# Kernel tuning notes

Hardware: AMD Instinct MI355X
Metric: run time of the kernel (lower is better)

Reference implementation:

```python
import jax, jax.numpy as jnp
import numpy as np
from math import sqrt

D_MODEL = 1024
D_HEAD = 128
TAU = 30.0
B, L = 8, 2048


def setup_inputs() -> dict:
    key = jax.random.key(0)
    k1, k2, k3, k4 = jax.random.split(key, 4)
    x = jax.random.normal(k1, (B, L, D_MODEL), dtype=jnp.float32)
    attention_mask = jnp.ones((B, L), dtype=jnp.int32)
    W_Q = jax.random.normal(k2, (D_HEAD, D_MODEL), dtype=jnp.float32)
    W_K = jax.random.normal(k3, (D_HEAD, D_MODEL), dtype=jnp.float32)
    W_V = jax.random.normal(k4, (D_HEAD, D_MODEL), dtype=jnp.float32)
    return {"input": x, "attention_mask": attention_mask, "W_Q": W_Q, "W_K": W_K, "W_V": W_V}


def reference(input, attention_mask, W_Q, W_K, W_V):
    # Single-head projections: [B, L, d_head]
    Q = input @ W_Q.T
    K = input @ W_K.T
    V = input @ W_V.T
    # Scaled scores: [B, L, L]
    S = jnp.einsum("bqd,bkd->bqk", Q, K) / sqrt(D_HEAD)
    # tanh soft-capping (mode == 'tanh-clipped')
    S = TAU * jnp.tanh(S)
    l = input.shape[1]
    # causal mask: strictly upper triangle -> -inf
    causal = jnp.triu(jnp.ones((l, l), dtype=bool), k=1)
    S = jnp.where(causal[None, :, :], -jnp.inf, S)
    # padding mask on keys: [B, 1, L]
    S = jnp.where(attention_mask[:, None, :] == 0, -jnp.inf, S)
    Attn = jax.nn.softmax(S, axis=-1)
    return Attn @ V
```

## Files before the change

### kernel.cpp

```cpp
#include <hip/hip_runtime.h>
#include <hip/hip_bf16.h>

#define BATCH  8
#define SEQ    2048
#define DMODEL 1024
#define DHEAD  128

typedef __attribute__((ext_vector_type(4))) float f32x4;
typedef __attribute__((ext_vector_type(4))) float f4;
typedef _Float16 f16;
typedef __attribute__((ext_vector_type(8))) _Float16 f16x8;
typedef __attribute__((ext_vector_type(8))) __bf16 bf16x8;
typedef __attribute__((ext_vector_type(16))) unsigned short u16x16;

__device__ __forceinline__ unsigned short f2bf(float f) {
    unsigned u = __builtin_bit_cast(unsigned, f);
    u += 0x7fffu + ((u >> 16) & 1u);
    return (unsigned short)(u >> 16);
}

#if __has_builtin(__builtin_amdgcn_exp2f)
#define EXP2(x) __builtin_amdgcn_exp2f(x)
#else
#define EXP2(x) exp2f(x)
#endif

__device__ __forceinline__ float fast_rcp(float x) {
#if __has_builtin(__builtin_amdgcn_rcpf)
    return __builtin_amdgcn_rcpf(x);
#else
    return 1.0f / x;
#endif
}

__device__ __forceinline__ void async_copy16(const void* g, void* l) {
    __builtin_amdgcn_global_load_lds(
        (const __attribute__((address_space(1))) unsigned int*)g,
        (__attribute__((address_space(3))) unsigned int*)l,
        16, 0, 0);
}

__global__ __launch_bounds__(256) void wsplit_kernel(
    const float* __restrict__ WQ, const float* __restrict__ WK,
    const float* __restrict__ WV, f16* __restrict__ Wsp)
{
    const int gid = blockIdx.x * 256 + threadIdx.x;
    const int row = gid & 127;
    const int hi  = (gid >> 7) & 3;
    const int ks  = (gid >> 9) & 31;
    const int mat = gid >> 14;
    const float* W = (mat < 2) ? WQ : (mat < 4) ? WK : WV;
    const float* src = W + (size_t)row * DMODEL + ks * 32 + hi * 8;
    f4 v0 = *(const f4*)src, v1 = *(const f4*)(src + 4);
    const bool lopart = (mat == 1 || mat == 3);
    f16x8 o;
    #pragma unroll
    for (int j = 0; j < 4; ++j) {
        f16 h0 = (f16)v0[j], h1 = (f16)v1[j];
        o[j]     = lopart ? (f16)(v0[j] - (float)h0) : h0;
        o[j + 4] = lopart ? (f16)(v1[j] - (float)h1) : h1;
    }
    *reinterpret_cast<f16x8*>(Wsp + (size_t)gid * 8) = o;
}

__global__ __launch_bounds__(256) void proj_kernel(
    const float* __restrict__ x, const f16* __restrict__ Wsp,
    f16* __restrict__ Qh, f16* __restrict__ Ql,
    f16* __restrict__ Kh, f16* __restrict__ Kl,
    unsigned short* __restrict__ Vtb)
{
    __shared__ float Xs[2][64][32];
    __shared__ f16 Wl[2][5][4][64][8];

    const int tid  = threadIdx.x;
    const int lane = tid & 63;
    const int w    = tid >> 6;
    const int lo   = lane & 15;
    const int hi   = lane >> 4;
    const int m0   = blockIdx.x * 64;
    const int bn   = blockIdx.y;

    f32x4 accQ[4] = {}, accK[4] = {}, accV[4] = {};

    const int r0 = (w * 2 + 0) * 8 + (lane >> 3);
    const int r1 = (w * 2 + 1) * 8 + (lane >> 3);
    const float* xsrc0 = x + (size_t)(m0 + r0) * DMODEL + (((lane & 7) ^ (r0 & 7)) << 2);
    const float* xsrc1 = x + (size_t)(m0 + r1) * DMODEL + (((lane & 7) ^ (r1 & 7)) << 2);
    const f16* wsrc0 = Wsp + (size_t)(w * 128 + bn * 64 + lane) * 8;

    auto stageX = [&](int ks, int buf) {
        async_copy16(xsrc0 + ks * 32, &Xs[buf][(w * 2 + 0) * 8][0]);
        async_copy16(xsrc1 + ks * 32, &Xs[buf][(w * 2 + 1) * 8][0]);
    };
    auto stageW = [&](int ks, int buf) {
        #pragma unroll
        for (int m = 0; m < 5; ++m)
            async_copy16(wsrc0 + (size_t)(m * 32 + ks) * 4096,
                         &Wl[buf][m][w][0][0]);
    };

    stageX(0, 0);
    stageW(0, 0);
    __syncthreads();

    for (int ks = 0; ks < 32; ++ks) {
        const int cur = ks & 1;
        if (ks < 31) { stageX(ks + 1, cur ^ 1); stageW(ks + 1, cur ^ 1); }

        f16x8 W5[5];
        #pragma unroll
        for (int m = 0; m < 5; ++m)
            W5[m] = *reinterpret_cast<const f16x8*>(&Wl[cur][m][hi][w * 16 + lo][0]);

        #pragma unroll
        for (int rb = 0; rb < 4; ++rb) {
            const int row = rb * 16 + lo;
            const float* xr = &Xs[cur][row][0];
            f4 a0 = *(const f4*)(xr + (((2 * hi)     ^ (row & 7)) << 2));
            f4 a1 = *(const f4*)(xr + (((2 * hi + 1) ^ (row & 7)) << 2));
            f16x8 ah, al;
            #pragma unroll
            for (int j = 0; j < 4; ++j) {
                f16 h0 = (f16)a0[j]; ah[j]     = h0; al[j]     = (f16)(a0[j] - (float)h0);
                f16 h1 = (f16)a1[j]; ah[j + 4] = h1; al[j + 4] = (f16)(a1[j] - (float)h1);
            }
            accQ[rb] = __builtin_amdgcn_mfma_f32_16x16x32_f16(ah, W5[0], accQ[rb], 0, 0, 0);
            accQ[rb] = __builtin_amdgcn_mfma_f32_16x16x32_f16(ah, W5[1], accQ[rb], 0, 0, 0);
            accQ[rb] = __builtin_amdgcn_mfma_f32_16x16x32_f16(al, W5[0], accQ[rb], 0, 0, 0);
            accK[rb] = __builtin_amdgcn_mfma_f32_16x16x32_f16(ah, W5[2], accK[rb], 0, 0, 0);
            accK[rb] = __builtin_amdgcn_mfma_f32_16x16x32_f16(ah, W5[3], accK[rb], 0, 0, 0);
            accK[rb] = __builtin_amdgcn_mfma_f32_16x16x32_f16(al, W5[2], accK[rb], 0, 0, 0);
            accV[rb] = __builtin_amdgcn_mfma_f32_16x16x32_f16(ah, W5[4], accV[rb], 0, 0, 0);
        }
        __syncthreads();
    }

    #pragma unroll
    for (int rb = 0; rb < 4; ++rb)
        #pragma unroll
        for (int r = 0; r < 4; ++r) {
            const int m = m0 + rb * 16 + hi * 4 + r;
            const int n = bn * 64 + w * 16 + lo;
            const size_t idx = (size_t)m * DHEAD + n;
            float vq = accQ[rb][r];
            f16 hq = (f16)vq;
            Qh[idx] = hq; Ql[idx] = (f16)(vq - (float)hq);
            float vk = accK[rb][r];
            f16 hk = (f16)vk;
            Kh[idx] = hk; Kl[idx] = (f16)(vk - (float)hk);
            const int bb = m >> 11, l = m & 2047;
            Vtb[((size_t)bb * DHEAD + n) * SEQ + l] = f2bf(accV[rb][r]);
        }
}

#define PART_STRIDE 8256
__global__ __launch_bounds__(512) void attn_kernel(
    const f16* __restrict__ Qh, const f16* __restrict__ Ql,
    const f16* __restrict__ Kh, const f16* __restrict__ Kl,
    const unsigned short* __restrict__ Vtb, const int* __restrict__ mask,
    float* __restrict__ part)
{
    __shared__ f16 Khs[2][64][136];
    __shared__ f16 Kls[2][64][136];
    __shared__ unsigned short Vs[2][128][72];
    __shared__ int Ms[2][64];
    __shared__ unsigned short Plds[8][16][40];

    const int tid  = threadIdx.x;
    const int lane = tid & 63;
    const int w    = tid >> 6;
    const int lo   = lane & 15;
    const int hi   = lane >> 4;
    const int wq   = w & 3;
    const int wk   = w >> 2;
    const int b    = blockIdx.x;
    const int qs   = 31 - (int)blockIdx.y;
    const int z    = blockIdx.z;
    const int qrow = qs * 64 + wq * 16;

    const float c2p = 0.25506061907448296f;
    const float c1  = -86.561702453337804f;

    f16x8 qh[4], ql[4];
    {
        const size_t off = ((size_t)(b * SEQ + qrow + lo)) * DHEAD + hi * 8;
        #pragma unroll
        for (int c = 0; c < 4; ++c) {
            qh[c] = *reinterpret_cast<const f16x8*>(Qh + off + c * 32);
            ql[c] = *reinterpret_cast<const f16x8*>(Ql + off + c * 32);
        }
    }

    const int krow = tid >> 3;
    const int kcol = (tid & 7) * 16;
    const int vrow = tid >> 2;
    const int vcol = (tid & 3) * 16;

    f16x8  rKh0, rKh1, rKl0, rKl1;
    u16x16 rV;
    int    rM = 0;

    auto load_tile = [&](int kb) {
        const size_t koff = ((size_t)(b * SEQ + kb + krow)) * DHEAD + kcol;
        rKh0 = *reinterpret_cast<const f16x8*>(Kh + koff);
        rKh1 = *reinterpret_cast<const f16x8*>(Kh + koff + 8);
        rKl0 = *reinterpret_cast<const f16x8*>(Kl + koff);
        rKl1 = *reinterpret_cast<const f16x8*>(Kl + koff + 8);
        rV   = *reinterpret_cast<const u16x16*>(Vtb + ((size_t)b * DHEAD + vrow) * SEQ + kb + vcol);
        if (tid < 64) rM = mask[b * SEQ + kb + tid];
    };
    auto write_tile = [&](int buf) {
        *reinterpret_cast<f16x8*>(&Khs[buf][krow][kcol])     = rKh0;
        *reinterpret_cast<f16x8*>(&Khs[buf][krow][kcol + 8]) = rKh1;
        *reinterpret_cast<f16x8*>(&Kls[buf][krow][kcol])     = rKl0;
        *reinterpret_cast<f16x8*>(&Kls[buf][krow][kcol + 8]) = rKl1;
        *reinterpret_cast<u16x16*>(&Vs[buf][vrow][vcol]) = rV;
        if (tid < 64) Ms[buf][tid] = rM;
    };

    load_tile(z * 64);
    write_tile(0);
    __syncthreads();

    f32x4 acc[8] = {};
    float rs[4] = {0.f, 0.f, 0.f, 0.f};

    int cnt = 0;
    for (int it = z; it <= qs; it += 2, ++cnt) {
        const int cur = cnt & 1;
        const bool havenext = (it + 2 <= qs);
        if (havenext) load_tile((it + 2) * 64);

        const int kb = it * 64 + wk * 32;
        if (kb <= qrow + 15) {
            #pragma unroll
            for (int h = 0; h < 2; ++h) {
                f32x4 s = {};
                #pragma unroll
                for (int c = 0; c < 4; ++c) {
                    f16x8 fkh = *reinterpret_cast<const f16x8*>(&Khs[cur][wk * 32 + h * 16 + lo][c * 32 + hi * 8]);
                    f16x8 fkl = *reinterpret_cast<const f16x8*>(&Kls[cur][wk * 32 + h * 16 + lo][c * 32 + hi * 8]);
                    s = __builtin_amdgcn_mfma_f32_16x16x32_f16(qh[c], fkh, s, 0, 0, 0);
                    s = __builtin_amdgcn_mfma_f32_16x16x32_f16(qh[c], fkl, s, 0, 0, 0);
                    s = __builtin_amdgcn_mfma_f32_16x16x32_f16(ql[c], fkh, s, 0, 0, 0);
                }
                const int key = kb + h * 16 + lo;
                const int mk  = Ms[cur][wk * 32 + h * 16 + lo];
                #pragma unroll
                for (int r = 0; r < 4; ++r) {
                    const int q = qrow + hi * 4 + r;
                    float t = EXP2(s[r] * c2p);
                    float p = EXP2(c1 * fast_rcp(t + 1.0f));
                    p = (key <= q && mk != 0) ? p : 0.0f;
                    rs[r] += p;
                    Plds[w][hi * 4 + r][h * 16 + lo] = f2bf(p);
                }
            }
            bf16x8 pa = *reinterpret_cast<const bf16x8*>(&Plds[w][lo][hi * 8]);
            #pragma unroll
            for (int dt = 0; dt < 8; ++dt) {
                bf16x8 vf = *reinterpret_cast<const bf16x8*>(&Vs[cur][dt * 16 + lo][wk * 32 + hi * 8]);
                acc[dt] = __builtin_amdgcn_mfma_f32_16x16x32_bf16(pa, vf, acc[dt], 0, 0, 0);
            }
        }

        if (havenext) write_tile(cur ^ 1);
        __syncthreads();
    }

    float* red = (float*)&Khs[0][0][0];
    if (wk == 1) {
        float* dst = red + ((size_t)wq * 64 + lane) * 36;
        #pragma unroll
        for (int dt = 0; dt < 8; ++dt)
            #pragma unroll
            for (int r = 0; r < 4; ++r) dst[dt * 4 + r] = acc[dt][r];
        #pragma unroll
        for (int r = 0; r < 4; ++r) dst[32 + r] = rs[r];
    }
    __syncthreads();
    if (wk == 0) {
        const float* src = red + ((size_t)wq * 64 + lane) * 36;
        #pragma unroll
        for (int dt = 0; dt < 8; ++dt)
            #pragma unroll
            for (int r = 0; r < 4; ++r) acc[dt][r] += src[dt * 4 + r];
        float rsum[4];
        #pragma unroll
        for (int r = 0; r < 4; ++r) {
            float v = rs[r] + src[32 + r];
            v += __shfl_xor(v, 1);
            v += __shfl_xor(v, 2);
            v += __shfl_xor(v, 4);
            v += __shfl_xor(v, 8);
            rsum[r] = v;
        }
        float* P = part + (((size_t)b * 32 + qs) * 2 + z) * PART_STRIDE;
        #pragma unroll
        for (int dt = 0; dt < 8; ++dt)
            #pragma unroll
            for (int r = 0; r < 4; ++r)
                P[(wq * 16 + hi * 4 + r) * 128 + dt * 16 + lo] = acc[dt][r];
        if (lo == 0)
            #pragma unroll
            for (int r = 0; r < 4; ++r)
                P[8192 + wq * 16 + hi * 4 + r] = rsum[r];
    }
}

__global__ __launch_bounds__(256) void merge_kernel(
    const float* __restrict__ part, float* __restrict__ out)
{
    const int gid = blockIdx.x * 256 + threadIdx.x;
    const int col = (gid & 31) * 4;
    const int q   = gid >> 5;
    const int b   = q >> 11, l = q & 2047;
    const int qs  = l >> 6, row = l & 63;
    const float* P0 = part + (((size_t)b * 32 + qs) * 2) * PART_STRIDE;
    const float* P1 = P0 + PART_STRIDE;
    f4 a0 = *(const f4*)(P0 + row * 128 + col);
    f4 a1 = *(const f4*)(P1 + row * 128 + col);
    float inv = fast_rcp(P0[8192 + row] + P1[8192 + row]);
    f4 o;
    #pragma unroll
    for (int j = 0; j < 4; ++j) o[j] = (a0[j] + a1[j]) * inv;
    *(f4*)(out + (size_t)q * 128 + col) = o;
}

extern "C" void kernel_launch(void* const* d_in, const int* in_sizes, int n_in,
                              void* d_out, int out_size, void* d_ws, size_t ws_size,
                              hipStream_t stream) {
    const float* x   = (const float*)d_in[0];
    const int*   msk = (const int*)d_in[1];
    const float* WQ  = (const float*)d_in[2];
    const float* WK  = (const float*)d_in[3];
    const float* WV  = (const float*)d_in[4];
    float* out = (float*)d_out;

    const size_t NE = (size_t)BATCH * SEQ * DHEAD;
    f16* Qh = (f16*)d_ws;
    f16* Ql = Qh + NE;
    f16* Kh = Ql + NE;
    f16* Kl = Kh + NE;
    unsigned short* Vtb = (unsigned short*)(Kl + NE);
    f16* Wsp = (f16*)(Vtb + NE);
    float* part = (float*)(Wsp + (size_t)5 * 32 * 4096);

    wsplit_kernel<<<320, 256, 0, stream>>>(WQ, WK, WV, Wsp);
    proj_kernel<<<dim3(BATCH * SEQ / 64, 2), 256, 0, stream>>>(x, Wsp, Qh, Ql, Kh, Kl, Vtb);
    attn_kernel<<<dim3(BATCH, 32, 2), 512, 0, stream>>>(Qh, Ql, Kh, Kl, Vtb, msk, part);
    merge_kernel<<<2048, 256, 0, stream>>>(part, out);
}
```

Baseline: 99.28 us.

## Triple-buffer projection operand staging with explicit vmcnt waits and single barrier

The projection kernel's shared-memory staging goes from double to triple buffering for X and the Q/K weight slices, prefetching two k-steps ahead. The V weight slice gets its own double buffer with one-step lookahead. The trailing __syncthreads is replaced by a manual s_waitcnt vmcnt plus s_barrier at the top of each iteration, so global loads can overlap more MFMA work. This adds LDS use, which may lower occupancy, and the hand-counted vmcnt value must match the number of outstanding copies.

```diff
diff --git a/kernel.cpp b/kernel.cpp
--- a/kernel.cpp
+++ b/kernel.cpp
@@ -69,8 +69,9 @@
     f16* __restrict__ Kh, f16* __restrict__ Kl,
     unsigned short* __restrict__ Vtb)
 {
-    __shared__ float Xs[2][64][32];
-    __shared__ f16 Wl[2][5][4][64][8];
+    __shared__ float Xs[3][64][32];
+    __shared__ f16 Wl[3][4][4][64][8];
+    __shared__ f16 Vl[2][4][64][8];
 
     const int tid  = threadIdx.x;
     const int lane = tid & 63;
@@ -88,34 +89,46 @@
     const float* xsrc1 = x + (size_t)(m0 + r1) * DMODEL + (((lane & 7) ^ (r1 & 7)) << 2);
     const f16* wsrc0 = Wsp + (size_t)(w * 128 + bn * 64 + lane) * 8;
 
-    auto stageX = [&](int ks, int buf) {
-        async_copy16(xsrc0 + ks * 32, &Xs[buf][(w * 2 + 0) * 8][0]);
-        async_copy16(xsrc1 + ks * 32, &Xs[buf][(w * 2 + 1) * 8][0]);
+    auto stage = [&](int ks, int s) {
+        async_copy16(xsrc0 + ks * 32, &Xs[s][(w * 2 + 0) * 8][0]);
+        async_copy16(xsrc1 + ks * 32, &Xs[s][(w * 2 + 1) * 8][0]);
+        #pragma unroll
+        for (int m = 0; m < 4; ++m)
+            async_copy16(wsrc0 + (size_t)(m * 32 + ks) * 4096,
+                         &Wl[s][m][w][0][0]);
     };
-    auto stageW = [&](int ks, int buf) {
-        #pragma unroll
-        for (int m = 0; m < 5; ++m)
-            async_copy16(wsrc0 + (size_t)(m * 32 + ks) * 4096,
-                         &Wl[buf][m][w][0][0]);
+    auto stageV = [&](int ks, int b) {
+        async_copy16(wsrc0 + (size_t)(4 * 32 + ks) * 4096,
+                     &Vl[b][w][0][0]);
     };
 
-    stageX(0, 0);
-    stageW(0, 0);
-    __syncthreads();
-
+    stageV(0, 0);
+    stage(0, 0);
+    stage(1, 1);
+
+    int cs = 0;
     for (int ks = 0; ks < 32; ++ks) {
-        const int cur = ks & 1;
-        if (ks < 31) { stageX(ks + 1, cur ^ 1); stageW(ks + 1, cur ^ 1); }
-
-        f16x8 W5[5];
-        #pragma unroll
-        for (int m = 0; m < 5; ++m)
-            W5[m] = *reinterpret_cast<const f16x8*>(&Wl[cur][m][hi][w * 16 + lo][0]);
+        if (ks < 31) {
+            asm volatile("s_waitcnt vmcnt(6) lgkmcnt(0)" ::: "memory");
+        } else {
+            asm volatile("s_waitcnt vmcnt(0) lgkmcnt(0)" ::: "memory");
+        }
+        __builtin_amdgcn_s_barrier();
+        __builtin_amdgcn_sched_barrier(0);
+
+        if (ks < 31) stageV(ks + 1, (ks + 1) & 1);
+        if (ks < 30) { int is = cs + 2; if (is >= 3) is -= 3; stage(ks + 2, is); }
+
+        f16x8 W4[4], WV5;
+        #pragma unroll
+        for (int m = 0; m < 4; ++m)
+            W4[m] = *reinterpret_cast<const f16x8*>(&Wl[cs][m][hi][w * 16 + lo][0]);
+        WV5 = *reinterpret_cast<const f16x8*>(&Vl[ks & 1][hi][w * 16 + lo][0]);
 
         #pragma unroll
         for (int rb = 0; rb < 4; ++rb) {
             const int row = rb * 16 + lo;
-            const float* xr = &Xs[cur][row][0];
+            const float* xr = &Xs[cs][row][0];
             f4 a0 = *(const f4*)(xr + (((2 * hi)     ^ (row & 7)) << 2));
             f4 a1 = *(const f4*)(xr + (((2 * hi + 1) ^ (row & 7)) << 2));
             f16x8 ah, al;
@@ -124,15 +137,16 @@
                 f16 h0 = (f16)a0[j]; ah[j]     = h0; al[j]     = (f16)(a0[j] - (float)h0);
                 f16 h1 = (f16)a1[j]; ah[j + 4] = h1; al[j + 4] = (f16)(a1[j] - (float)h1);
             }
-            accQ[rb] = __builtin_amdgcn_mfma_f32_16x16x32_f16(ah, W5[0], accQ[rb], 0, 0, 0);
-            accQ[rb] = __builtin_amdgcn_mfma_f32_16x16x32_f16(ah, W5[1], accQ[rb], 0, 0, 0);
-            accQ[rb] = __builtin_amdgcn_mfma_f32_16x16x32_f16(al, W5[0], accQ[rb], 0, 0, 0);
-            accK[rb] = __builtin_amdgcn_mfma_f32_16x16x32_f16(ah, W5[2], accK[rb], 0, 0, 0);
-            accK[rb] = __builtin_amdgcn_mfma_f32_16x16x32_f16(ah, W5[3], accK[rb], 0, 0, 0);
-            accK[rb] = __builtin_amdgcn_mfma_f32_16x16x32_f16(al, W5[2], accK[rb], 0, 0, 0);
-            accV[rb] = __builtin_amdgcn_mfma_f32_16x16x32_f16(ah, W5[4], accV[rb], 0, 0, 0);
-        }
-        __syncthreads();
+            accQ[rb] = __builtin_amdgcn_mfma_f32_16x16x32_f16(ah, W4[0], accQ[rb], 0, 0, 0);
+            accQ[rb] = __builtin_amdgcn_mfma_f32_16x16x32_f16(ah, W4[1], accQ[rb], 0, 0, 0);
+            accQ[rb] = __builtin_amdgcn_mfma_f32_16x16x32_f16(al, W4[0], accQ[rb], 0, 0, 0);
+            accK[rb] = __builtin_amdgcn_mfma_f32_16x16x32_f16(ah, W4[2], accK[rb], 0, 0, 0);
+            accK[rb] = __builtin_amdgcn_mfma_f32_16x16x32_f16(ah, W4[3], accK[rb], 0, 0, 0);
+            accK[rb] = __builtin_amdgcn_mfma_f32_16x16x32_f16(al, W4[2], accK[rb], 0, 0, 0);
+            accV[rb] = __builtin_amdgcn_mfma_f32_16x16x32_f16(ah, WV5, accV[rb], 0, 0, 0);
+        }
+
+        cs = (cs == 2) ? 0 : cs + 1;
     }
 
     #pragma unroll
```

Measured after the change: 102.2 us. 1.03x slower.
